# Kernel optimization log

Hardware: AMD Instinct MI355X
Metric: run time of the kernel (lower is better)

The kernel has to match this reference:

```python
import jax, jax.numpy as jnp
import numpy as np

DIM = 2048
N_HEADS = 16
QK_NOPE = 128
QK_ROPE = 64
V_DIM = 128
QK_DIM = QK_NOPE + QK_ROPE  # 192
B, S = 2, 2048


def setup_inputs() -> dict:
    key = jax.random.key(0)
    ks = jax.random.split(key, 6)
    x = jax.random.normal(ks[0], (B, S, DIM), dtype=jnp.float32)
    # rotary angles: theta[j] = 10000^{-2j/d}, angle[p, j] = p * theta[j]
    inv_freq = 1.0 / (10000.0 ** (np.arange(0, QK_ROPE, 2, dtype=np.float32) / QK_ROPE))
    freqs = jnp.asarray(np.arange(S, dtype=np.float32)[:, None] * inv_freq[None, :])  # [S, QK_ROPE//2]
    # additive causal mask
    mask = jnp.where(jnp.tril(jnp.ones((S, S), dtype=bool)), 0.0, -1e9).astype(jnp.float32)
    sc = 1.0 / np.sqrt(DIM)
    wq = jax.random.normal(ks[1], (DIM, N_HEADS * QK_DIM), dtype=jnp.float32) * sc
    wk = jax.random.normal(ks[2], (DIM, N_HEADS * QK_DIM), dtype=jnp.float32) * sc
    wv = jax.random.normal(ks[3], (DIM, N_HEADS * V_DIM), dtype=jnp.float32) * sc
    wo = jax.random.normal(ks[4], (N_HEADS * V_DIM, DIM), dtype=jnp.float32) * (1.0 / np.sqrt(N_HEADS * V_DIM))
    return {"x": x, "start_pos": 0, "freqs": freqs, "mask": mask,
            "wq": wq, "wk": wk, "wv": wv, "wo": wo}


def _apply_rope(t, freqs):
    # t: [B, S, H, D_rope]; freqs: [S, D_rope//2] angles
    b, s, h, d = t.shape
    tr = t.reshape(b, s, h, d // 2, 2)
    cos = jnp.cos(freqs)[None, :, None, :]
    sin = jnp.sin(freqs)[None, :, None, :]
    out = jnp.stack([tr[..., 0] * cos - tr[..., 1] * sin,
                     tr[..., 0] * sin + tr[..., 1] * cos], axis=-1)
    return out.reshape(b, s, h, d)


def reference(x, start_pos, freqs, mask, wq, wk, wv, wo):
    b, s, _ = x.shape
    xq = x @ wq  # [B,S,H*QK_DIM]
    xk = x @ wk
    xv = (x @ wv).reshape(b, s, N_HEADS, V_DIM)
    qnope, qrope = jnp.split(xq, [N_HEADS * QK_NOPE], axis=-1)
    knope, krope = jnp.split(xk, [N_HEADS * QK_NOPE], axis=-1)
    qnope = qnope.reshape(b, s, N_HEADS, QK_NOPE)
    knope = knope.reshape(b, s, N_HEADS, QK_NOPE)
    qrope = _apply_rope(qrope.reshape(b, s, N_HEADS, QK_ROPE), freqs)
    krope = _apply_rope(krope.reshape(b, s, N_HEADS, QK_ROPE), freqs)
    q = jnp.concatenate([qnope, qrope], axis=-1)  # [B,S,H,QK_DIM]
    k = jnp.concatenate([knope, krope], axis=-1)
    scale = 1.0 / jnp.sqrt(jnp.asarray(QK_DIM, dtype=q.dtype))
    scores = jnp.einsum('bqhd,bkhd->bhqk', q, k) * scale
    scores = scores + mask[None, None, :, :]
    attn = jax.nn.softmax(scores.astype(jnp.float32), axis=-1).astype(scores.dtype)
    out = jnp.einsum('bhqk,bkhd->bqhd', attn, xv)  # [B,S,H,V_DIM]
    out = out.reshape(b, s, N_HEADS * V_DIM)
    return out @ wo
```

## Files before the change

### kernel.cpp

```cpp
#include <hip/hip_runtime.h>
#include <hip/hip_bf16.h>

typedef __attribute__((ext_vector_type(4))) float f32x4;
typedef __attribute__((ext_vector_type(8))) short s16x8;
typedef unsigned int u32;
typedef unsigned short u16;

#define GLDS16(gp, lp) __builtin_amdgcn_global_load_lds(                         \
    (const __attribute__((address_space(1))) u32*)(gp),                          \
    (__attribute__((address_space(3))) u32*)(lp), 16, 0, 0)
#define VMCNT4 asm volatile("s_waitcnt vmcnt(4)" ::: "memory")
#define VMCNT8 asm volatile("s_waitcnt vmcnt(8)" ::: "memory")
#define VMCNT0 asm volatile("s_waitcnt vmcnt(0)" ::: "memory")
#define LGKM0  asm volatile("s_waitcnt lgkmcnt(0)" ::: "memory")
#define SBAR   __builtin_amdgcn_sched_barrier(0)

__device__ __forceinline__ u16 f2bf(float f) {
    u32 u = __builtin_bit_cast(u32, f);
    u32 r = (u + 0x7FFFu + ((u >> 16) & 1u)) >> 16;
    return (u16)r;
}
__device__ __forceinline__ float bf2f(u16 h) {
    u32 u = ((u32)h) << 16;
    return __builtin_bit_cast(float, u);
}

__global__ __launch_bounds__(256) void conv_f32_bf16(const float4* __restrict__ in,
                                                     ushort4* __restrict__ out, int n4) {
    int i = blockIdx.x * 256 + threadIdx.x;
    if (i < n4) {
        float4 v = in[i];
        ushort4 o;
        o.x = f2bf(v.x); o.y = f2bf(v.y); o.z = f2bf(v.z); o.w = f2bf(v.w);
        out[i] = o;
    }
}

__global__ __launch_bounds__(256) void wtrans(const float* __restrict__ in,
                                              u16* __restrict__ out, int K, int N) {
    __shared__ float tile[32][33];
    int n0 = blockIdx.x * 32, k0 = blockIdx.y * 32;
    int tx = threadIdx.x & 31, ty = threadIdx.x >> 5;
#pragma unroll
    for (int i = 0; i < 4; ++i)
        tile[ty + i * 8][tx] = in[(size_t)(k0 + ty + i * 8) * N + n0 + tx];
    __syncthreads();
#pragma unroll
    for (int i = 0; i < 4; ++i) {
        int n = ty + i * 8;
        out[(size_t)(n0 + n) * K + k0 + tx] = f2bf(tile[tx][n]);
    }
}

__global__ __launch_bounds__(512, 2) void gemm_qkv(const u16* __restrict__ A,
                                                   const u16* __restrict__ W,
                                                   u16* __restrict__ Qh,
                                                   u16* __restrict__ Kh,
                                                   u16* __restrict__ Vn) {
    __shared__ __align__(16) u16 lds[4][2][256 * 32];
    const int tid = threadIdx.x, lane = tid & 63, wid = tid >> 6;
    const int l15 = lane & 15, l4 = lane >> 4;
    const int id = blockIdx.x;
    const int nt = ((id & 7) << 2) + ((id >> 3) & 3);
    const int mt = id >> 5;
    const int bm0 = mt << 8, bn0 = nt << 8;
    const int wr = wid >> 2, wc = wid & 3;
    f32x4 acc[8][4] = {};

    auto stage = [&](int step) {
        const int kc = step << 5;
        u16* La = lds[step & 3][0];
        u16* Lb = lds[step & 3][1];
#pragma unroll
        for (int j = 0; j < 2; ++j) {
            int c = j * 512 + tid;
            int row = c >> 2, s2 = c & 3;
            int cs = s2 ^ ((row >> 1) & 3);
            GLDS16(A + (size_t)(bm0 + row) * 2048 + kc + cs * 8,
                   (char*)La + (j * 512 + wid * 64) * 16);
        }
#pragma unroll
        for (int j = 0; j < 2; ++j) {
            int c = j * 512 + tid;
            int row = c >> 2, s2 = c & 3;
            int cs = s2 ^ ((row >> 1) & 3);
            GLDS16(W + (size_t)(bn0 + row) * 2048 + kc + cs * 8,
                   (char*)Lb + (j * 512 + wid * 64) * 16);
        }
    };

    stage(0); stage(1); stage(2);
    VMCNT8;
    __builtin_amdgcn_s_barrier();
    SBAR;

    const int swz = (l4 * 16) ^ (((l15 >> 1) & 3) << 4);
    for (int t = 0; t < 64; ++t) {
        const u16* Ab = lds[t & 3][0];
        const u16* Bb = lds[t & 3][1];
        s16x8 af[8], bf[4];
#pragma unroll
        for (int m = 0; m < 8; ++m)
            af[m] = *(const s16x8*)((const char*)Ab + (wr * 128 + m * 16 + l15) * 64 + swz);
#pragma unroll
        for (int n = 0; n < 4; ++n)
            bf[n] = *(const s16x8*)((const char*)Bb + (wc * 64 + n * 16 + l15) * 64 + swz);
        __builtin_amdgcn_s_setprio(1);
#pragma unroll
        for (int m = 0; m < 8; ++m)
#pragma unroll
            for (int n = 0; n < 4; ++n)
                acc[m][n] = __builtin_amdgcn_mfma_f32_16x16x32_bf16(af[m], bf[n],
                                                                    acc[m][n], 0, 0, 0);
        __builtin_amdgcn_s_setprio(0);
        if (t < 63) {
            SBAR;
            LGKM0;
            if (t >= 62) { VMCNT0; } else { VMCNT4; }
            __builtin_amdgcn_s_barrier();
            SBAR;
            if (t + 3 < 64) stage(t + 3);
            SBAR;
        }
    }

#pragma unroll
    for (int m = 0; m < 8; ++m)
#pragma unroll
        for (int n = 0; n < 4; ++n)
#pragma unroll
            for (int r = 0; r < 4; ++r) {
                int row = bm0 + wr * 128 + m * 16 + l4 * 4 + r;
                int c = bn0 + wc * 64 + n * 16 + l15;
                float v = acc[m][n][r];
                if (bn0 >= 6144) {
                    Vn[(size_t)row * 2048 + (c - 6144)] = f2bf(v);
                } else {
                    u16* dst = (bn0 >= 3072) ? Kh : Qh;
                    int cc = (bn0 >= 3072) ? c - 3072 : c;
                    int b = row >> 11, s = row & 2047;
                    int h, d;
                    if (cc < 2048) { h = cc >> 7; d = cc & 127; }
                    else { int mm = cc - 2048; h = mm >> 6; d = 128 + (mm & 63); }
                    dst[(((size_t)b * 16 + h) * 2048 + s) * 192 + d] = f2bf(v);
                }
            }
}

__global__ __launch_bounds__(256) void gemm_bt_f32(const u16* __restrict__ A,
                                                   const u16* __restrict__ Bt,
                                                   float* __restrict__ C,
                                                   int M, int N, int K) {
    __shared__ __align__(16) u16 As[128 * 64];
    __shared__ __align__(16) u16 Bs[128 * 64];
    const int tid = threadIdx.x, lane = tid & 63, wid = tid >> 6;
    const int l15 = lane & 15, l4 = lane >> 4;
    const int bm0 = blockIdx.y << 7, bn0 = blockIdx.x << 7;
    const int wr = wid >> 1, wc = wid & 1;
    f32x4 acc[4][4] = {};
    const int nk = K >> 6;
    for (int t = 0; t < nk; ++t) {
        const int k0 = t << 6;
#pragma unroll
        for (int i = 0; i < 4; ++i) {
            int c = i * 256 + tid;
            int row = c >> 3, c8 = c & 7;
            GLDS16(A + (size_t)(bm0 + row) * K + k0 + c8 * 8,
                   (char*)As + (i * 256 + wid * 64) * 16);
        }
#pragma unroll
        for (int i = 0; i < 4; ++i) {
            int c = i * 256 + tid;
            int row = c >> 3, c8 = c & 7;
            GLDS16(Bt + (size_t)(bn0 + row) * K + k0 + c8 * 8,
                   (char*)Bs + (i * 256 + wid * 64) * 16);
        }
        __syncthreads();
#pragma unroll
        for (int kk = 0; kk < 64; kk += 32) {
            s16x8 af[4], bfr[4];
#pragma unroll
            for (int m = 0; m < 4; ++m)
                af[m] = *(const s16x8*)(As + (wr * 64 + m * 16 + l15) * 64 + kk + l4 * 8);
#pragma unroll
            for (int n = 0; n < 4; ++n)
                bfr[n] = *(const s16x8*)(Bs + (wc * 64 + n * 16 + l15) * 64 + kk + l4 * 8);
#pragma unroll
            for (int m = 0; m < 4; ++m)
#pragma unroll
                for (int n = 0; n < 4; ++n)
                    acc[m][n] = __builtin_amdgcn_mfma_f32_16x16x32_bf16(af[m], bfr[n],
                                                                        acc[m][n], 0, 0, 0);
        }
        __syncthreads();
    }
#pragma unroll
    for (int m = 0; m < 4; ++m)
#pragma unroll
        for (int n = 0; n < 4; ++n)
#pragma unroll
            for (int r = 0; r < 4; ++r) {
                int row = bm0 + wr * 64 + m * 16 + l4 * 4 + r;
                int col = bn0 + wc * 64 + n * 16 + l15;
                C[(size_t)row * N + col] = acc[m][n][r];
            }
}

__global__ __launch_bounds__(256) void rope_inplace(u16* __restrict__ T,
                                                    const float* __restrict__ freqs) {
    int idx = blockIdx.x * 256 + threadIdx.x;
    int j = idx & 31, s = (idx >> 5) & 2047, bh = idx >> 16;
    float ang = freqs[s * 32 + j];
    float c = cosf(ang), sn = sinf(ang);
    u32* p = (u32*)(T + ((size_t)bh * 2048 + s) * 192 + 128) + j;
    u32 v = *p;
    float t0 = bf2f((u16)(v & 0xffff)), t1 = bf2f((u16)(v >> 16));
    float o0 = t0 * c - t1 * sn;
    float o1 = t0 * sn + t1 * c;
    *p = (u32)f2bf(o0) | ((u32)f2bf(o1) << 16);
}

__global__ __launch_bounds__(256) void vtrans(const u16* __restrict__ Vn,
                                              u16* __restrict__ Vt) {
    __shared__ u16 tile[32][33];
    int s0 = blockIdx.x * 32, d0 = blockIdx.y * 32, bh = blockIdx.z;
    int b = bh >> 4, h = bh & 15;
    int tx = threadIdx.x & 31, ty = threadIdx.x >> 5;
#pragma unroll
    for (int i = 0; i < 4; ++i) {
        int s = ty + i * 8;
        tile[s][tx] = Vn[((size_t)b * 2048 + s0 + s) * 2048 + h * 128 + d0 + tx];
    }
    __syncthreads();
#pragma unroll
    for (int i = 0; i < 4; ++i) {
        int d = ty + i * 8;
        Vt[((size_t)bh * 128 + d0 + d) * 2048 + s0 + tx] = tile[tx][d];
    }
}

__global__ __launch_bounds__(256) void attn_fwd3(const u16* __restrict__ Qh,
                                                 const u16* __restrict__ Kh,
                                                 const u16* __restrict__ Vt,
                                                 u16* __restrict__ AO) {
    __shared__ __align__(16) u16 Ks[64 * 192];
    __shared__ __align__(16) u16 Vs[128 * 64];
    __shared__ __align__(16) u16 Ps[4][32 * 64];
    const int tid = threadIdx.x, lane = tid & 63, wid = tid >> 6;
    const int l15 = lane & 15, l4 = lane >> 4;
    const int id = blockIdx.x;
    const int bh = id & 31;
    const int qt = 15 - (id >> 5);
    const int q0 = qt << 7;
    const u16* Qb = Qh + ((size_t)bh * 2048 + q0 + wid * 32) * 192;
    const u16* Kb = Kh + (size_t)bh * 2048 * 192;
    const u16* Vb = Vt + (size_t)bh * 128 * 2048;

    s16x8 aq[2][6];
#pragma unroll
    for (int qg = 0; qg < 2; ++qg)
#pragma unroll
        for (int dk = 0; dk < 6; ++dk)
            aq[qg][dk] = *(const s16x8*)(Qb + (size_t)(qg * 16 + l15) * 192 + dk * 32 + l4 * 8);

    f32x4 acc[2][8] = {};
    float mrow[2][4], lpart[2][4];
#pragma unroll
    for (int qg = 0; qg < 2; ++qg)
#pragma unroll
        for (int r = 0; r < 4; ++r) { mrow[qg][r] = -1e30f; lpart[qg][r] = 0.f; }
    const float scale = 0.07216878364870322f;

    const int ntile = (qt + 1) << 1;
    for (int t = 0; t < ntile; ++t) {
        const int k0 = t << 6;
#pragma unroll
        for (int i = 0; i < 6; ++i) {
            int c = i * 256 + tid;
            int row = (u32)c / 24u, cc = c - row * 24;
            int cs = (cc & 24) | ((cc ^ row) & 7);
            GLDS16(Kb + (size_t)(k0 + row) * 192 + cs * 8,
                   (char*)Ks + (i * 256 + wid * 64) * 16);
        }
#pragma unroll
        for (int i = 0; i < 4; ++i) {
            int c = i * 256 + tid;
            int d = c >> 3, cc = c & 7;
            int cs = cc ^ (d & 7);
            GLDS16(Vb + (size_t)d * 2048 + k0 + cs * 8,
                   (char*)Vs + (i * 256 + wid * 64) * 16);
        }
        __syncthreads();

        if (q0 + wid * 32 + 31 >= k0) {
            f32x4 sc[2][4];
#pragma unroll
            for (int qg = 0; qg < 2; ++qg)
#pragma unroll
                for (int kg = 0; kg < 4; ++kg) sc[qg][kg] = f32x4{0.f, 0.f, 0.f, 0.f};
            __builtin_amdgcn_s_setprio(1);
#pragma unroll
            for (int dk = 0; dk < 6; ++dk) {
                s16x8 bk[4];
#pragma unroll
                for (int kg = 0; kg < 4; ++kg) {
                    int row = kg * 16 + l15;
                    int byt = (row * 384 + dk * 64 + l4 * 16) ^ ((row & 7) << 4);
                    bk[kg] = *(const s16x8*)((const char*)Ks + byt);
                }
#pragma unroll
                for (int qg = 0; qg < 2; ++qg)
#pragma unroll
                    for (int kg = 0; kg < 4; ++kg)
                        sc[qg][kg] = __builtin_amdgcn_mfma_f32_16x16x32_bf16(
                            aq[qg][dk], bk[kg], sc[qg][kg], 0, 0, 0);
            }
            __builtin_amdgcn_s_setprio(0);

            u16* Pw = Ps[wid];
#pragma unroll
            for (int qg = 0; qg < 2; ++qg) {
                const int qrow = q0 + wid * 32 + qg * 16 + l4 * 4;
                const bool domask = (k0 + 63 > qrow);
                float p[4][4], tm[4];
#pragma unroll
                for (int r = 0; r < 4; ++r) tm[r] = -1e30f;
#pragma unroll
                for (int kg = 0; kg < 4; ++kg)
#pragma unroll
                    for (int r = 0; r < 4; ++r) {
                        float v = sc[qg][kg][r] * scale;
                        if (domask && (k0 + kg * 16 + l15 > qrow + r)) v = -1e30f;
                        p[kg][r] = v;
                        tm[r] = fmaxf(tm[r], v);
                    }
#pragma unroll
                for (int off = 1; off < 16; off <<= 1)
#pragma unroll
                    for (int r = 0; r < 4; ++r)
                        tm[r] = fmaxf(tm[r], __shfl_xor(tm[r], off, 64));
                float mn[4];
                bool resc = false;
#pragma unroll
                for (int r = 0; r < 4; ++r) {
                    mn[r] = (tm[r] <= mrow[qg][r] + 8.f) ? mrow[qg][r] : tm[r];
                    resc |= (mn[r] > mrow[qg][r]);
                }
                if (__any(resc)) {
#pragma unroll
                    for (int r = 0; r < 4; ++r) {
                        float scl = __expf(mrow[qg][r] - mn[r]);
                        mrow[qg][r] = mn[r];
                        lpart[qg][r] *= scl;
#pragma unroll
                        for (int db = 0; db < 8; ++db) acc[qg][db][r] *= scl;
                    }
                }
#pragma unroll
                for (int kg = 0; kg < 4; ++kg)
#pragma unroll
                    for (int r = 0; r < 4; ++r) {
                        p[kg][r] = __expf(p[kg][r] - mrow[qg][r]);
                        lpart[qg][r] += p[kg][r];
                    }
#pragma unroll
                for (int kg = 0; kg < 4; ++kg)
#pragma unroll
                    for (int r = 0; r < 4; ++r) {
                        int row = qg * 16 + l4 * 4 + r;
                        int byt = ((row * 64 + kg * 16 + l15) * 2) ^ ((row & 7) << 4);
                        *(u16*)((char*)Pw + byt) = f2bf(p[kg][r]);
                    }
            }

            __builtin_amdgcn_s_setprio(1);
#pragma unroll
            for (int kk = 0; kk < 2; ++kk) {
                s16x8 ap[2];
#pragma unroll
                for (int qg = 0; qg < 2; ++qg) {
                    int row = qg * 16 + l15;
                    int byt = ((row * 64 + kk * 32 + l4 * 8) * 2) ^ ((row & 7) << 4);
                    ap[qg] = *(const s16x8*)((const char*)Pw + byt);
                }
#pragma unroll
                for (int db = 0; db < 8; ++db) {
                    int row = db * 16 + l15;
                    int byt = (row * 128 + kk * 64 + l4 * 16) ^ ((row & 7) << 4);
                    s16x8 bv = *(const s16x8*)((const char*)Vs + byt);
#pragma unroll
                    for (int qg = 0; qg < 2; ++qg)
                        acc[qg][db] = __builtin_amdgcn_mfma_f32_16x16x32_bf16(
                            ap[qg], bv, acc[qg][db], 0, 0, 0);
                }
            }
            __builtin_amdgcn_s_setprio(0);
        }
        __syncthreads();
    }

#pragma unroll
    for (int off = 1; off < 16; off <<= 1)
#pragma unroll
        for (int qg = 0; qg < 2; ++qg)
#pragma unroll
            for (int r = 0; r < 4; ++r)
                lpart[qg][r] += __shfl_xor(lpart[qg][r], off, 64);

    const int b = bh >> 4, h = bh & 15;
#pragma unroll
    for (int qg = 0; qg < 2; ++qg) {
        float inv[4];
#pragma unroll
        for (int r = 0; r < 4; ++r) inv[r] = 1.f / lpart[qg][r];
#pragma unroll
        for (int db = 0; db < 8; ++db)
#pragma unroll
            for (int r = 0; r < 4; ++r) {
                int row = q0 + wid * 32 + qg * 16 + l4 * 4 + r;
                AO[((size_t)b * 2048 + row) * 2048 + h * 128 + db * 16 + l15] =
                    f2bf(acc[qg][db][r] * inv[r]);
            }
    }
}

extern "C" void kernel_launch(void* const* d_in, const int* in_sizes, int n_in,
                              void* d_out, int out_size, void* d_ws, size_t ws_size,
                              hipStream_t stream) {
    const float* x     = (const float*)d_in[0];
    const float* freqs = (const float*)d_in[2];
    const float* wq    = (const float*)d_in[4];
    const float* wk    = (const float*)d_in[5];
    const float* wv    = (const float*)d_in[6];
    const float* wo    = (const float*)d_in[7];
    float* out = (float*)d_out;

    char* ws = (char*)d_ws;
    u16* xb   = (u16*)(ws + 0);
    u16* WT   = (u16*)(ws + 16777216);
    u16* woT  = (u16*)(ws + 50331648);
    u16* Qh   = (u16*)(ws + 58720256);
    u16* Kh   = (u16*)(ws + 83886080);
    u16* Vn   = (u16*)(ws + 109051904);
    u16* Vt   = (u16*)(ws + 125829120);
    u16* AO   = (u16*)(ws + 142606336);

    conv_f32_bf16<<<8192, 256, 0, stream>>>((const float4*)x, (ushort4*)xb, 2097152);
    wtrans<<<dim3(96, 64), 256, 0, stream>>>(wq, WT, 2048, 3072);
    wtrans<<<dim3(96, 64), 256, 0, stream>>>(wk, WT + (size_t)3072 * 2048, 2048, 3072);
    wtrans<<<dim3(64, 64), 256, 0, stream>>>(wv, WT + (size_t)6144 * 2048, 2048, 2048);
    wtrans<<<dim3(64, 64), 256, 0, stream>>>(wo, woT, 2048, 2048);
    gemm_qkv<<<dim3(512), 512, 0, stream>>>(xb, WT, Qh, Kh, Vn);
    rope_inplace<<<8192, 256, 0, stream>>>(Qh, freqs);
    rope_inplace<<<8192, 256, 0, stream>>>(Kh, freqs);
    vtrans<<<dim3(64, 4, 32), 256, 0, stream>>>(Vn, Vt);
    attn_fwd3<<<dim3(512), 256, 0, stream>>>(Qh, Kh, Vt, AO);
    gemm_bt_f32<<<dim3(16, 32), 256, 0, stream>>>(AO, woT, out, 4096, 2048, 2048);
}
```

Measured before the change: 364.0 us.

## Split QKV GEMM main loop into two phases interleaving loads with MFMA

```diff
diff --git a/kernel.cpp b/kernel.cpp
--- a/kernel.cpp
+++ b/kernel.cpp
@@ -67,10 +67,9 @@
     const int wr = wid >> 2, wc = wid & 3;
     f32x4 acc[8][4] = {};
 
-    auto stage = [&](int step) {
+    auto stageA = [&](int step) {
         const int kc = step << 5;
         u16* La = lds[step & 3][0];
-        u16* Lb = lds[step & 3][1];
 #pragma unroll
         for (int j = 0; j < 2; ++j) {
             int c = j * 512 + tid;
@@ -79,6 +78,10 @@
             GLDS16(A + (size_t)(bm0 + row) * 2048 + kc + cs * 8,
                    (char*)La + (j * 512 + wid * 64) * 16);
         }
+    };
+    auto stageB = [&](int step) {
+        const int kc = step << 5;
+        u16* Lb = lds[step & 3][1];
 #pragma unroll
         for (int j = 0; j < 2; ++j) {
             int c = j * 512 + tid;
@@ -89,7 +92,7 @@
         }
     };
 
-    stage(0); stage(1); stage(2);
+    stageA(0); stageB(0); stageA(1); stageB(1); stageA(2); stageB(2);
     VMCNT8;
     __builtin_amdgcn_s_barrier();
     SBAR;
@@ -98,30 +101,48 @@
     for (int t = 0; t < 64; ++t) {
         const u16* Ab = lds[t & 3][0];
         const u16* Bb = lds[t & 3][1];
-        s16x8 af[8], bf[4];
-#pragma unroll
-        for (int m = 0; m < 8; ++m)
-            af[m] = *(const s16x8*)((const char*)Ab + (wr * 128 + m * 16 + l15) * 64 + swz);
+        s16x8 af0[4], bfr[4];
 #pragma unroll
         for (int n = 0; n < 4; ++n)
-            bf[n] = *(const s16x8*)((const char*)Bb + (wc * 64 + n * 16 + l15) * 64 + swz);
+            bfr[n] = *(const s16x8*)((const char*)Bb + (wc * 64 + n * 16 + l15) * 64 + swz);
+#pragma unroll
+        for (int m = 0; m < 4; ++m)
+            af0[m] = *(const s16x8*)((const char*)Ab + (wr * 128 + m * 16 + l15) * 64 + swz);
+        if (t + 3 < 64) stageA(t + 3);
+        SBAR;
+        __builtin_amdgcn_s_barrier();
+        LGKM0;
+        SBAR;
         __builtin_amdgcn_s_setprio(1);
 #pragma unroll
-        for (int m = 0; m < 8; ++m)
+        for (int m = 0; m < 4; ++m)
 #pragma unroll
             for (int n = 0; n < 4; ++n)
-                acc[m][n] = __builtin_amdgcn_mfma_f32_16x16x32_bf16(af[m], bf[n],
+                acc[m][n] = __builtin_amdgcn_mfma_f32_16x16x32_bf16(af0[m], bfr[n],
                                                                     acc[m][n], 0, 0, 0);
         __builtin_amdgcn_s_setprio(0);
+        SBAR;
+        s16x8 af1[4];
+#pragma unroll
+        for (int m = 0; m < 4; ++m)
+            af1[m] = *(const s16x8*)((const char*)Ab + (wr * 128 + (m + 4) * 16 + l15) * 64 + swz);
+        if (t + 3 < 64) stageB(t + 3);
         if (t < 63) {
+            if (t < 61) { VMCNT8; } else if (t == 61) { VMCNT4; } else { VMCNT0; }
             SBAR;
-            LGKM0;
-            if (t >= 62) { VMCNT0; } else { VMCNT4; }
             __builtin_amdgcn_s_barrier();
-            SBAR;
-            if (t + 3 < 64) stage(t + 3);
-            SBAR;
-        }
+        }
+        LGKM0;
+        SBAR;
+        __builtin_amdgcn_s_setprio(1);
+#pragma unroll
+        for (int m = 0; m < 4; ++m)
+#pragma unroll
+            for (int n = 0; n < 4; ++n)
+                acc[m + 4][n] = __builtin_amdgcn_mfma_f32_16x16x32_bf16(af1[m], bfr[n],
+                                                                        acc[m + 4][n], 0, 0, 0);
+        __builtin_amdgcn_s_setprio(0);
+        SBAR;
     }
 
 #pragma unroll
```

After: 361.0 us. Within noise of the previous version (-0.8%).

## Double-buffer LDS fragments in registers for the QKV GEMM main loop

Applied to the files above, without the earlier changes.

```diff
diff --git a/kernel.cpp b/kernel.cpp
--- a/kernel.cpp
+++ b/kernel.cpp
@@ -12,6 +12,7 @@
 #define VMCNT4 asm volatile("s_waitcnt vmcnt(4)" ::: "memory")
 #define VMCNT8 asm volatile("s_waitcnt vmcnt(8)" ::: "memory")
 #define VMCNT0 asm volatile("s_waitcnt vmcnt(0)" ::: "memory")
+#define LGKM12 asm volatile("s_waitcnt lgkmcnt(12)" ::: "memory")
 #define LGKM0  asm volatile("s_waitcnt lgkmcnt(0)" ::: "memory")
 #define SBAR   __builtin_amdgcn_sched_barrier(0)
 
@@ -67,10 +68,9 @@
     const int wr = wid >> 2, wc = wid & 3;
     f32x4 acc[8][4] = {};
 
-    auto stage = [&](int step) {
+    auto stageA = [&](int step) {
         const int kc = step << 5;
         u16* La = lds[step & 3][0];
-        u16* Lb = lds[step & 3][1];
 #pragma unroll
         for (int j = 0; j < 2; ++j) {
             int c = j * 512 + tid;
@@ -79,6 +79,10 @@
             GLDS16(A + (size_t)(bm0 + row) * 2048 + kc + cs * 8,
                    (char*)La + (j * 512 + wid * 64) * 16);
         }
+    };
+    auto stageB = [&](int step) {
+        const int kc = step << 5;
+        u16* Lb = lds[step & 3][1];
 #pragma unroll
         for (int j = 0; j < 2; ++j) {
             int c = j * 512 + tid;
@@ -89,40 +93,58 @@
         }
     };
 
-    stage(0); stage(1); stage(2);
+    const int swz = (l4 * 16) ^ (((l15 >> 1) & 3) << 4);
+    s16x8 fA[12], fB[12];
+
+#define LDFRAG(T1, F)                                                          \
+    {                                                                          \
+        const u16* Ab_ = lds[(T1) & 3][0];                                     \
+        const u16* Bb_ = lds[(T1) & 3][1];                                     \
+        _Pragma("unroll")                                                      \
+        for (int m_ = 0; m_ < 8; ++m_)                                         \
+            F[m_] = *(const s16x8*)((const char*)Ab_ +                         \
+                                    (wr * 128 + m_ * 16 + l15) * 64 + swz);    \
+        _Pragma("unroll")                                                      \
+        for (int n_ = 0; n_ < 4; ++n_)                                         \
+            F[8 + n_] = *(const s16x8*)((const char*)Bb_ +                     \
+                                        (wc * 64 + n_ * 16 + l15) * 64 + swz); \
+    }
+
+#define QKV_STEP(T, CUR, NXT)                                                  \
+    {                                                                          \
+        const int t_ = (T);                                                    \
+        if (t_ == 62) { VMCNT0; } else if (t_ < 62) { VMCNT4; }                \
+        SBAR;                                                                  \
+        __builtin_amdgcn_s_barrier();                                          \
+        SBAR;                                                                  \
+        if (t_ < 63) LDFRAG(t_ + 1, NXT);                                      \
+        if (t_ < 61) { stageA(t_ + 3); stageB(t_ + 3); }                       \
+        SBAR;                                                                  \
+        if (t_ < 63) { LGKM12; } else { LGKM0; }                               \
+        SBAR;                                                                  \
+        __builtin_amdgcn_s_setprio(1);                                         \
+        _Pragma("unroll")                                                      \
+        for (int m_ = 0; m_ < 8; ++m_)                                         \
+            _Pragma("unroll")                                                  \
+            for (int n_ = 0; n_ < 4; ++n_)                                     \
+                acc[m_][n_] = __builtin_amdgcn_mfma_f32_16x16x32_bf16(         \
+                    CUR[m_], CUR[8 + n_], acc[m_][n_], 0, 0, 0);               \
+        __builtin_amdgcn_s_setprio(0);                                         \
+        SBAR;                                                                  \
+    }
+
+    stageA(0); stageB(0); stageA(1); stageB(1); stageA(2); stageB(2);
     VMCNT8;
     __builtin_amdgcn_s_barrier();
     SBAR;
-
-    const int swz = (l4 * 16) ^ (((l15 >> 1) & 3) << 4);
-    for (int t = 0; t < 64; ++t) {
-        const u16* Ab = lds[t & 3][0];
-        const u16* Bb = lds[t & 3][1];
-        s16x8 af[8], bf[4];
-#pragma unroll
-        for (int m = 0; m < 8; ++m)
-            af[m] = *(const s16x8*)((const char*)Ab + (wr * 128 + m * 16 + l15) * 64 + swz);
-#pragma unroll
-        for (int n = 0; n < 4; ++n)
-            bf[n] = *(const s16x8*)((const char*)Bb + (wc * 64 + n * 16 + l15) * 64 + swz);
-        __builtin_amdgcn_s_setprio(1);
-#pragma unroll
-        for (int m = 0; m < 8; ++m)
-#pragma unroll
-            for (int n = 0; n < 4; ++n)
-                acc[m][n] = __builtin_amdgcn_mfma_f32_16x16x32_bf16(af[m], bf[n],
-                                                                    acc[m][n], 0, 0, 0);
-        __builtin_amdgcn_s_setprio(0);
-        if (t < 63) {
-            SBAR;
-            LGKM0;
-            if (t >= 62) { VMCNT0; } else { VMCNT4; }
-            __builtin_amdgcn_s_barrier();
-            SBAR;
-            if (t + 3 < 64) stage(t + 3);
-            SBAR;
-        }
-    }
+    LDFRAG(0, fA);
+
+    for (int t = 0; t < 64; t += 2) {
+        QKV_STEP(t, fA, fB);
+        QKV_STEP(t + 1, fB, fA);
+    }
+#undef QKV_STEP
+#undef LDFRAG
 
 #pragma unroll
     for (int m = 0; m < 8; ++m)
```

After: 363.8 us. About the same (-0.0%).

## Restructure QKV GEMM mainloop into K=64 double-buffered half-tiles with interleaved loads

Applied to the files above, without the earlier changes.

```diff
diff --git a/kernel.cpp b/kernel.cpp
--- a/kernel.cpp
+++ b/kernel.cpp
@@ -10,8 +10,8 @@
     (const __attribute__((address_space(1))) u32*)(gp),                          \
     (__attribute__((address_space(3))) u32*)(lp), 16, 0, 0)
 #define VMCNT4 asm volatile("s_waitcnt vmcnt(4)" ::: "memory")
-#define VMCNT8 asm volatile("s_waitcnt vmcnt(8)" ::: "memory")
 #define VMCNT0 asm volatile("s_waitcnt vmcnt(0)" ::: "memory")
+#define LGKM8  asm volatile("s_waitcnt lgkmcnt(8)" ::: "memory")
 #define LGKM0  asm volatile("s_waitcnt lgkmcnt(0)" ::: "memory")
 #define SBAR   __builtin_amdgcn_sched_barrier(0)
 
@@ -57,7 +57,7 @@
                                                    u16* __restrict__ Qh,
                                                    u16* __restrict__ Kh,
                                                    u16* __restrict__ Vn) {
-    __shared__ __align__(16) u16 lds[4][2][256 * 32];
+    __shared__ __align__(16) u16 S[2][2][2][128 * 64];
     const int tid = threadIdx.x, lane = tid & 63, wid = tid >> 6;
     const int l15 = lane & 15, l4 = lane >> 4;
     const int id = blockIdx.x;
@@ -67,62 +67,89 @@
     const int wr = wid >> 2, wc = wid & 3;
     f32x4 acc[8][4] = {};
 
-    auto stage = [&](int step) {
-        const int kc = step << 5;
-        u16* La = lds[step & 3][0];
-        u16* Lb = lds[step & 3][1];
+    auto stageH = [&](int mat, int tt, int h) {
+        const int kc = tt << 6, p = tt & 1;
+        const u16* G = mat ? W : A;
+        const int rbase = (mat ? bn0 : bm0) + (h << 7);
+        u16* Ld = S[mat][p][h];
 #pragma unroll
         for (int j = 0; j < 2; ++j) {
             int c = j * 512 + tid;
-            int row = c >> 2, s2 = c & 3;
-            int cs = s2 ^ ((row >> 1) & 3);
-            GLDS16(A + (size_t)(bm0 + row) * 2048 + kc + cs * 8,
-                   (char*)La + (j * 512 + wid * 64) * 16);
-        }
-#pragma unroll
-        for (int j = 0; j < 2; ++j) {
-            int c = j * 512 + tid;
-            int row = c >> 2, s2 = c & 3;
-            int cs = s2 ^ ((row >> 1) & 3);
-            GLDS16(W + (size_t)(bn0 + row) * 2048 + kc + cs * 8,
-                   (char*)Lb + (j * 512 + wid * 64) * 16);
+            int row = c >> 3, ch = c & 7;
+            int cs = ch ^ (row & 7);
+            GLDS16(G + (size_t)(rbase + row) * 2048 + kc + cs * 8,
+                   (char*)Ld + (j * 512 + wid * 64) * 16);
         }
     };
 
-    stage(0); stage(1); stage(2);
-    VMCNT8;
+    s16x8 af[2][2], bfr[4][2];
+
+#define RDA(P, I)                                                              \
+    _Pragma("unroll") for (int mm = 0; mm < 2; ++mm)                           \
+    _Pragma("unroll") for (int kk = 0; kk < 2; ++kk) {                         \
+        int r7 = ((I) * 2 + mm) * 16 + l15;                                    \
+        int byt = r7 * 128 + (((kk * 4 + l4) ^ (r7 & 7)) << 4);                \
+        af[mm][kk] = *(const s16x8*)((const char*)S[0][P][wr] + byt);          \
+    }
+#define RDB(P)                                                                 \
+    _Pragma("unroll") for (int n = 0; n < 4; ++n)                              \
+    _Pragma("unroll") for (int kk = 0; kk < 2; ++kk) {                         \
+        int r7 = (wc & 1) * 64 + n * 16 + l15;                                 \
+        int byt = r7 * 128 + (((kk * 4 + l4) ^ (r7 & 7)) << 4);                \
+        bfr[n][kk] = *(const s16x8*)((const char*)S[1][P][wc >> 1] + byt);     \
+    }
+#define MF(I)                                                                  \
+    __builtin_amdgcn_s_setprio(1);                                             \
+    _Pragma("unroll") for (int mm = 0; mm < 2; ++mm)                           \
+    _Pragma("unroll") for (int n = 0; n < 4; ++n)                              \
+    _Pragma("unroll") for (int kk = 0; kk < 2; ++kk)                           \
+        acc[(I) * 2 + mm][n] = __builtin_amdgcn_mfma_f32_16x16x32_bf16(        \
+            af[mm][kk], bfr[n][kk], acc[(I) * 2 + mm][n], 0, 0, 0);            \
+    __builtin_amdgcn_s_setprio(0);
+
+    stageH(0, 0, 0); stageH(0, 0, 1); stageH(1, 0, 0); stageH(1, 0, 1);
+    stageH(0, 1, 0); stageH(0, 1, 1);
+    VMCNT4;
     __builtin_amdgcn_s_barrier();
     SBAR;
 
-    const int swz = (l4 * 16) ^ (((l15 >> 1) & 3) << 4);
-    for (int t = 0; t < 64; ++t) {
-        const u16* Ab = lds[t & 3][0];
-        const u16* Bb = lds[t & 3][1];
-        s16x8 af[8], bf[4];
-#pragma unroll
-        for (int m = 0; m < 8; ++m)
-            af[m] = *(const s16x8*)((const char*)Ab + (wr * 128 + m * 16 + l15) * 64 + swz);
-#pragma unroll
-        for (int n = 0; n < 4; ++n)
-            bf[n] = *(const s16x8*)((const char*)Bb + (wc * 64 + n * 16 + l15) * 64 + swz);
-        __builtin_amdgcn_s_setprio(1);
-#pragma unroll
-        for (int m = 0; m < 8; ++m)
-#pragma unroll
-            for (int n = 0; n < 4; ++n)
-                acc[m][n] = __builtin_amdgcn_mfma_f32_16x16x32_bf16(af[m], bf[n],
-                                                                    acc[m][n], 0, 0, 0);
-        __builtin_amdgcn_s_setprio(0);
-        if (t < 63) {
+    for (int t = 0; t < 32; ++t) {
+        const int p = t & 1;
+        RDB(p); RDA(p, 0);
+        if (t == 0) stageH(1, 1, 0);
+        else if (t < 31) stageH(0, t + 1, 0);
+        LGKM8; SBAR;
+        __builtin_amdgcn_s_barrier();
+        LGKM0; SBAR;
+        MF(0); SBAR;
+        __builtin_amdgcn_s_barrier();
+        RDA(p, 1);
+        if (t == 0) stageH(1, 1, 1);
+        else if (t < 31) stageH(0, t + 1, 1);
+        __builtin_amdgcn_s_barrier();
+        LGKM0; SBAR;
+        MF(1); SBAR;
+        __builtin_amdgcn_s_barrier();
+        RDA(p, 2);
+        if (t < 30) stageH(1, t + 2, 0);
+        __builtin_amdgcn_s_barrier();
+        LGKM0; SBAR;
+        MF(2); SBAR;
+        __builtin_amdgcn_s_barrier();
+        RDA(p, 3);
+        if (t < 30) stageH(1, t + 2, 1);
+        __builtin_amdgcn_s_barrier();
+        LGKM0; SBAR;
+        MF(3); SBAR;
+        if (t < 31) {
+            if (t < 30) { VMCNT4; } else { VMCNT0; }
             SBAR;
-            LGKM0;
-            if (t >= 62) { VMCNT0; } else { VMCNT4; }
-            __builtin_amdgcn_s_barrier();
-            SBAR;
-            if (t + 3 < 64) stage(t + 3);
-            SBAR;
-        }
-    }
+        }
+        __builtin_amdgcn_s_barrier();
+    }
+#undef RDA
+#undef RDB
+#undef MF
 
 #pragma unroll
     for (int m = 0; m < 8; ++m)
```

Measured after the change: 359.0 us. Within noise of the previous version (-1.4%).
